# Performance work log

Hardware: AMD Instinct MI355X
Metric: run time of the kernel (lower is better)

Reference implementation:

```python
import jax, jax.numpy as jnp
import numpy as np

B, S, D = 2, 2048, 2048
E, K, F = 8, 2, 4096
EPS_LN = 1e-5
EPS_AUX = 1e-9


def setup_inputs() -> dict:
    key = jax.random.key(0)
    ks = jax.random.split(key, 12)
    s_d = 1.0 / np.sqrt(D)
    s_f = 1.0 / np.sqrt(F)
    return {
        "x": jax.random.normal(ks[0], (B, S, D), dtype=jnp.float32),
        # router LayerNorm
        "ln_gamma": jnp.ones((D,), jnp.float32),
        "ln_beta": jnp.zeros((D,), jnp.float32),
        # router MLP: Linear(D,D) -> ReLU -> Linear(D,E)
        "rW1": jax.random.uniform(ks[1], (D, D), jnp.float32, -s_d, s_d),
        "rb1": jnp.zeros((D,), jnp.float32),
        "rW2": jax.random.uniform(ks[2], (D, E), jnp.float32, -s_d, s_d),
        "rb2": jnp.zeros((E,), jnp.float32),
        # experts: per-expert FFN D -> F -> D
        "We1": jax.random.uniform(ks[3], (E, D, F), jnp.float32, -s_d, s_d),
        "be1": jnp.zeros((E, F), jnp.float32),
        "We2": jax.random.uniform(ks[4], (E, F, D), jnp.float32, -s_f, s_f),
        "be2": jnp.zeros((E, D), jnp.float32),
    }


def _layer_norm(x, gamma, beta):
    mu = jnp.mean(x, axis=-1, keepdims=True)
    var = jnp.mean(jnp.square(x - mu), axis=-1, keepdims=True)
    return (x - mu) * jax.lax.rsqrt(var + EPS_LN) * gamma + beta


def reference(x, ln_gamma, ln_beta, rW1, rb1, rW2, rb2, We1, be1, We2, be2):
    # --- BaseRouter ---
    x_norm = _layer_norm(x, ln_gamma, ln_beta)
    h = jax.nn.relu(jnp.einsum("bsd,de->bse", x_norm, rW1) + rb1)
    router_logits = jnp.einsum("bsd,de->bse", h, rW2) + rb2  # [B,S,E]
    router_probs = jax.nn.softmax(router_logits, axis=-1)

    top_k_probs, top_k_indices = jax.lax.top_k(router_probs, K)  # [B,S,K]
    top_k_probs = top_k_probs / jnp.sum(top_k_probs, axis=-1, keepdims=True)

    # aux load-balance loss (detached in original via .item())
    p_mean = jnp.mean(router_probs, axis=(0, 1))  # [E]
    aux_loss = jnp.sum(p_mean * jnp.log(p_mean * E + EPS_AUX))

    # --- dispatch / combine weights: scatter top-k probs to [B,S,E] ---
    one_hot = jax.nn.one_hot(top_k_indices, E, dtype=x.dtype)  # [B,S,K,E]
    combine = jnp.einsum("bske,bsk->bse", one_hot, top_k_probs)  # [B,S,E]

    # --- experts: dense per-expert FFN, weighted combine ---
    eh = jax.nn.relu(jnp.einsum("bsd,edf->ebsf", x, We1) + be1[:, None, None, :])
    ey = jnp.einsum("ebsf,efd->ebsd", eh, We2) + be2[:, None, None, :]
    out = jnp.einsum("ebsd,bse->bsd", ey, combine)

    return out, aux_loss
```

## Files before the change

kernel.cpp:

```cpp
#include <hip/hip_runtime.h>
#include <hip/hip_bf16.h>

#define NTOK 4096
#define DIM  2048
#define NEXP 8
#define FDIM 4096
#define NPAIR 8192

typedef __attribute__((ext_vector_type(4))) float     f32x4;
typedef __attribute__((ext_vector_type(8))) short     s16x8;
typedef __attribute__((ext_vector_type(4))) short     s16x4;
typedef __attribute__((ext_vector_type(8))) _Float16  f16x8;
typedef __attribute__((ext_vector_type(4))) _Float16  f16x4;

#define DEVI static __device__ __forceinline__

DEVI void gl2lds(const void* g, void* l) {
  __builtin_amdgcn_global_load_lds((const __attribute__((address_space(1))) unsigned int*)g,
                                   (__attribute__((address_space(3))) unsigned int*)l, 16, 0, 0);
}

DEVI float bf2f(unsigned short s) {
  unsigned int u = ((unsigned int)s) << 16; float f; __builtin_memcpy(&f, &u, 4); return f;
}
DEVI unsigned short f2bf(float f) {
  __hip_bfloat16 h = __float2bfloat16(f); unsigned short s; __builtin_memcpy(&s, &h, 2); return s;
}
DEVI float wredsum(float v) {
#pragma unroll
  for (int o = 32; o > 0; o >>= 1) v += __shfl_xor(v, o);
  return v;
}

__global__ __launch_bounds__(256) void ln_conv_kernel(
    const float* __restrict__ x, const float* __restrict__ gamma, const float* __restrict__ beta,
    _Float16* __restrict__ xh, _Float16* __restrict__ xl, unsigned short* __restrict__ xbf)
{
  int tok = blockIdx.x;
  int tid = threadIdx.x, lane = tid & 63, wv = tid >> 6;
  const float* xr = x + (size_t)tok * DIM;
  float v[8];
  *(float4*)(v)     = *(const float4*)(xr + tid * 8);
  *(float4*)(v + 4) = *(const float4*)(xr + tid * 8 + 4);
  float s = v[0]+v[1]+v[2]+v[3]+v[4]+v[5]+v[6]+v[7];
  __shared__ float red[4];
  s = wredsum(s);
  if (lane == 0) red[wv] = s;
  __syncthreads();
  float mu = (red[0]+red[1]+red[2]+red[3]) * (1.f / DIM);
  __syncthreads();
  float s2 = 0.f;
#pragma unroll
  for (int j = 0; j < 8; j++) { float d = v[j] - mu; s2 += d * d; }
  s2 = wredsum(s2);
  if (lane == 0) red[wv] = s2;
  __syncthreads();
  float var = (red[0]+red[1]+red[2]+red[3]) * (1.f / DIM);
  float rs = 1.0f / sqrtf(var + 1e-5f);

  float4 g0 = *(const float4*)(gamma + tid*8), g1 = *(const float4*)(gamma + tid*8 + 4);
  float4 b0 = *(const float4*)(beta  + tid*8), b1 = *(const float4*)(beta  + tid*8 + 4);
  float gg[8] = {g0.x,g0.y,g0.z,g0.w,g1.x,g1.y,g1.z,g1.w};
  float bb[8] = {b0.x,b0.y,b0.z,b0.w,b1.x,b1.y,b1.z,b1.w};
  f16x8 vh, vl; s16x8 vb;
#pragma unroll
  for (int j = 0; j < 8; j++) {
    float xn = (v[j] - mu) * rs * gg[j] + bb[j];
    _Float16 h = (_Float16)xn;
    vh[j] = h;
    vl[j] = (_Float16)((xn - (float)h) * 4096.f);
    vb[j] = (short)f2bf(v[j]);
  }
  *(f16x8*)(xh + (size_t)tok*DIM + tid*8) = vh;
  *(f16x8*)(xl + (size_t)tok*DIM + tid*8) = vl;
  *(s16x8*)(xbf + (size_t)tok*DIM + tid*8) = vb;
}

__global__ __launch_bounds__(256) void transpose_bf16_kernel(
    const float* __restrict__ src, unsigned short* __restrict__ dst, int R, int C)
{
  src += (size_t)blockIdx.z * R * C;
  dst += (size_t)blockIdx.z * R * C;
  __shared__ float tile[64][65];
  int r0 = blockIdx.y * 64, c0 = blockIdx.x * 64;
  int tx = threadIdx.x & 15, ty = threadIdx.x >> 4;
#pragma unroll
  for (int i = 0; i < 4; i++) {
    float4 v = *(const float4*)(src + (size_t)(r0 + ty*4 + i) * C + c0 + tx*4);
    tile[ty*4+i][tx*4+0] = v.x; tile[ty*4+i][tx*4+1] = v.y;
    tile[ty*4+i][tx*4+2] = v.z; tile[ty*4+i][tx*4+3] = v.w;
  }
  __syncthreads();
#pragma unroll
  for (int i = 0; i < 4; i++) {
    int c = c0 + ty*4 + i;
    s16x4 o;
    o[0] = (short)f2bf(tile[tx*4+0][ty*4+i]); o[1] = (short)f2bf(tile[tx*4+1][ty*4+i]);
    o[2] = (short)f2bf(tile[tx*4+2][ty*4+i]); o[3] = (short)f2bf(tile[tx*4+3][ty*4+i]);
    *(s16x4*)(dst + (size_t)c * R + r0 + tx*4) = o;
  }
}

__global__ __launch_bounds__(256) void transpose_f16split_kernel(
    const float* __restrict__ src, _Float16* __restrict__ dh, _Float16* __restrict__ dl, int R, int C)
{
  __shared__ float tile[64][65];
  int r0 = blockIdx.y * 64, c0 = blockIdx.x * 64;
  int tx = threadIdx.x & 15, ty = threadIdx.x >> 4;
#pragma unroll
  for (int i = 0; i < 4; i++) {
    float4 v = *(const float4*)(src + (size_t)(r0 + ty*4 + i) * C + c0 + tx*4);
    tile[ty*4+i][tx*4+0] = v.x; tile[ty*4+i][tx*4+1] = v.y;
    tile[ty*4+i][tx*4+2] = v.z; tile[ty*4+i][tx*4+3] = v.w;
  }
  __syncthreads();
#pragma unroll
  for (int i = 0; i < 4; i++) {
    int c = c0 + ty*4 + i;
    f16x4 oh, ol;
#pragma unroll
    for (int j = 0; j < 4; j++) {
      float f = tile[tx*4+j][ty*4+i];
      _Float16 h = (_Float16)f;
      oh[j] = h;
      ol[j] = (_Float16)((f - (float)h) * 4096.f);
    }
    *(f16x4*)(dh + (size_t)c * R + r0 + tx*4) = oh;
    *(f16x4*)(dl + (size_t)c * R + r0 + tx*4) = ol;
  }
}

#define R_TA 10240
#define R_TB 5120
__global__ __launch_bounds__(256) void router_gemm_kernel(
    const _Float16* __restrict__ Ah, const _Float16* __restrict__ Al,
    const _Float16* __restrict__ Bh, const _Float16* __restrict__ Bl,
    const float* __restrict__ bias, float* __restrict__ Cout)
{
  __shared__ char lds[2*R_TA + 2*R_TB];
  char* lAh = lds;             char* lAl = lds + R_TA;
  char* lBh = lds + 2*R_TA;    char* lBl = lds + 2*R_TA + R_TB;
  const int K = DIM;
  int m0 = blockIdx.y * 128, n0 = blockIdx.x * 64;
  int tid = threadIdx.x, lane = tid & 63, wv = tid >> 6;
  int wm = wv >> 1, wn = wv & 1;

  const char* srcAh[3]; const char* srcAl[3];
  const char* srcBh[2]; const char* srcBl[2];
  {
    int i = 0;
    for (int c = wv; c < 10; c += 4, i++) {
      int doff = c*1024 + lane*16;
      int row = doff / 80; int b = doff - row*80; if (b >= 64) b = 0;
      srcAh[i] = (const char*)(Ah + (size_t)(m0+row)*K) + b;
      srcAl[i] = (const char*)(Al + (size_t)(m0+row)*K) + b;
    }
    i = 0;
    for (int c = wv; c < 5; c += 4, i++) {
      int doff = c*1024 + lane*16;
      int row = doff / 80; int b = doff - row*80; if (b >= 64) b = 0;
      srcBh[i] = (const char*)(Bh + (size_t)(n0+row)*K) + b;
      srcBl[i] = (const char*)(Bl + (size_t)(n0+row)*K) + b;
    }
  }

  f32x4 acc1[4][2], acc2[4][2];
#pragma unroll
  for (int mb = 0; mb < 4; mb++)
#pragma unroll
    for (int nb = 0; nb < 2; nb++) {
      acc1[mb][nb] = (f32x4){0.f,0.f,0.f,0.f};
      acc2[mb][nb] = (f32x4){0.f,0.f,0.f,0.f};
    }

  for (int kt = 0; kt < K/32; kt++) {
    {
      int i = 0;
      for (int c = wv; c < 10; c += 4, i++) {
        gl2lds(srcAh[i], lAh + c*1024);
        gl2lds(srcAl[i], lAl + c*1024);
        srcAh[i] += 64; srcAl[i] += 64;
      }
      i = 0;
      for (int c = wv; c < 5; c += 4, i++) {
        gl2lds(srcBh[i], lBh + c*1024);
        gl2lds(srcBl[i], lBl + c*1024);
        srcBh[i] += 64; srcBl[i] += 64;
      }
    }
    __syncthreads();
    int kb = (lane >> 4) * 16;
    f16x8 ah[4], al[4], bh[2], bl[2];
#pragma unroll
    for (int mb = 0; mb < 4; mb++) {
      int r = wm*64 + mb*16 + (lane & 15);
      ah[mb] = *(const f16x8*)(lAh + r*80 + kb);
      al[mb] = *(const f16x8*)(lAl + r*80 + kb);
    }
#pragma unroll
    for (int nb = 0; nb < 2; nb++) {
      int r = wn*32 + nb*16 + (lane & 15);
      bh[nb] = *(const f16x8*)(lBh + r*80 + kb);
      bl[nb] = *(const f16x8*)(lBl + r*80 + kb);
    }
#pragma unroll
    for (int mb = 0; mb < 4; mb++)
#pragma unroll
      for (int nb = 0; nb < 2; nb++) {
        acc1[mb][nb] = __builtin_amdgcn_mfma_f32_16x16x32_f16(ah[mb], bh[nb], acc1[mb][nb], 0,0,0);
        acc2[mb][nb] = __builtin_amdgcn_mfma_f32_16x16x32_f16(ah[mb], bl[nb], acc2[mb][nb], 0,0,0);
        acc2[mb][nb] = __builtin_amdgcn_mfma_f32_16x16x32_f16(al[mb], bh[nb], acc2[mb][nb], 0,0,0);
      }
    __syncthreads();
  }
#pragma unroll
  for (int mb = 0; mb < 4; mb++)
#pragma unroll
    for (int nb = 0; nb < 2; nb++) {
      int col = n0 + wn*32 + nb*16 + (lane & 15);
      float bv = bias[col];
#pragma unroll
      for (int r = 0; r < 4; r++) {
        int m = m0 + wm*64 + mb*16 + (lane >> 4)*4 + r;
        float hval = acc1[mb][nb][r] + acc2[mb][nb][r] * (1.f/4096.f) + bv;
        Cout[(size_t)m*DIM + col] = fmaxf(hval, 0.f);
      }
    }
}

__global__ __launch_bounds__(256) void router_logits_kernel(
    const float* __restrict__ h, const float* __restrict__ rW2, const float* __restrict__ rb2,
    float* __restrict__ probs,
    int* __restrict__ eid, float* __restrict__ wts)
{
  int lane = threadIdx.x & 63, wv = threadIdx.x >> 6;
  int tok = blockIdx.x * 4 + wv;
  const float* hr = h + (size_t)tok * DIM;
  float lg[8] = {0,0,0,0,0,0,0,0};
#pragma unroll
  for (int j = 0; j < 8; j++) {
    int k = j * 256 + lane * 4;
    float4 hv = *(const float4*)(hr + k);
    float hv4[4] = {hv.x, hv.y, hv.z, hv.w};
#pragma unroll
    for (int r = 0; r < 4; r++) {
      const float4* w4 = (const float4*)(rW2 + (size_t)(k + r) * NEXP);
      float4 wa = w4[0], wb = w4[1];
      lg[0] += hv4[r]*wa.x; lg[1] += hv4[r]*wa.y; lg[2] += hv4[r]*wa.z; lg[3] += hv4[r]*wa.w;
      lg[4] += hv4[r]*wb.x; lg[5] += hv4[r]*wb.y; lg[6] += hv4[r]*wb.z; lg[7] += hv4[r]*wb.w;
    }
  }
#pragma unroll
  for (int e = 0; e < 8; e++) {
#pragma unroll
    for (int o = 32; o > 0; o >>= 1) lg[e] += __shfl_xor(lg[e], o);
  }
  if (lane == 0) {
    float l[8], p[8];
    float m = -1e30f;
#pragma unroll
    for (int e = 0; e < 8; e++) { l[e] = lg[e] + rb2[e]; m = fmaxf(m, l[e]); }
    float s = 0.f;
#pragma unroll
    for (int e = 0; e < 8; e++) { p[e] = expf(l[e] - m); s += p[e]; }
    float inv = 1.f / s;
#pragma unroll
    for (int e = 0; e < 8; e++) { p[e] *= inv; probs[(size_t)tok*8 + e] = p[e]; }
    int i0 = 0;
#pragma unroll
    for (int e = 1; e < 8; e++) if (p[e] > p[i0]) i0 = e;
    int i1 = (i0 == 0) ? 1 : 0;
#pragma unroll
    for (int e = 0; e < 8; e++) if (e != i0 && p[e] > p[i1]) i1 = e;
    float denom = 1.f / (p[i0] + p[i1]);
    eid[tok*2+0] = i0; eid[tok*2+1] = i1;
    wts[tok*2+0] = p[i0]*denom; wts[tok*2+1] = p[i1]*denom;
  }
}

__global__ __launch_bounds__(256) void router_sort_kernel(
    const int* __restrict__ eid, const float* __restrict__ probs,
    int* __restrict__ cnt, int* __restrict__ basep,
    int* __restrict__ tokenlist, int* __restrict__ pairslot,
    float* __restrict__ aux_out)
{
  __shared__ int hist[256][8];
  __shared__ float wsum[4][8];
  __shared__ int bl[8];
  __shared__ int lcnt[8];
  int t = threadIdx.x, lane = t & 63, wv = t >> 6;

  int me[32];
  {
    const int4* ep = (const int4*)(eid + t * 32);
#pragma unroll
    for (int q = 0; q < 8; q++) {
      int4 v = ep[q];
      me[q*4+0] = v.x; me[q*4+1] = v.y; me[q*4+2] = v.z; me[q*4+3] = v.w;
    }
  }
#pragma unroll
  for (int e = 0; e < 8; e++) {
    int ce = 0;
#pragma unroll
    for (int i = 0; i < 32; i++) ce += (me[i] == e) ? 1 : 0;
    hist[t][e] = ce;
  }

  float part[8] = {0,0,0,0,0,0,0,0};
  for (int i = 0; i < 16; i++) {
    const float4* p4 = (const float4*)(probs + (size_t)(t*16 + i) * 8);
    float4 a = p4[0], b = p4[1];
    part[0]+=a.x; part[1]+=a.y; part[2]+=a.z; part[3]+=a.w;
    part[4]+=b.x; part[5]+=b.y; part[6]+=b.z; part[7]+=b.w;
  }
#pragma unroll
  for (int e = 0; e < 8; e++) {
#pragma unroll
    for (int o = 32; o > 0; o >>= 1) part[e] += __shfl_xor(part[e], o);
  }
  if (lane == 0) {
#pragma unroll
    for (int e = 0; e < 8; e++) wsum[wv][e] = part[e];
  }
  __syncthreads();

  if (t < 8) {
    int running = 0;
    for (int i = 0; i < 256; i++) { int tmp = hist[i][t]; hist[i][t] = running; running += tmp; }
    lcnt[t] = running;
  }
  __syncthreads();
  if (t == 0) {
    int b = 0; float aux = 0.f;
#pragma unroll
    for (int e = 0; e < 8; e++) {
      int ce = lcnt[e];
      bl[e] = b; basep[e] = b; cnt[e] = ce; b += ce;
      float pm = (wsum[0][e]+wsum[1][e]+wsum[2][e]+wsum[3][e]) * (1.f / NTOK);
      aux += pm * logf(pm * 8.f + 1e-9f);
    }
    *aux_out = aux;
  }
  __syncthreads();

#pragma unroll
  for (int i = 0; i < 32; i++) {
    int e = me[i];
    int r = 0;
#pragma unroll
    for (int j = 0; j < i; j++) r += (me[j] == e) ? 1 : 0;
    int slot = bl[e] + hist[t][e] + r;
    int pair = t*32 + i;
    tokenlist[slot] = pair >> 1;
    pairslot[pair] = slot;
  }
}

#define E_TILE 18432
template<int MODE>
__global__ __launch_bounds__(256) void expert_gemm_kernel(
    const unsigned short* __restrict__ Abase,
    const unsigned short* __restrict__ Bbase,
    const float* __restrict__ bias,
    unsigned short* __restrict__ Cout,
    const int* __restrict__ cnt, const int* __restrict__ basep,
    const int* __restrict__ tokenlist)
{
  const int K = (MODE == 1) ? DIM : FDIM;
  const int N = (MODE == 1) ? FDIM : DIM;
  int e = blockIdx.y >> 5, mt = blockIdx.y & 31;
  int ne = cnt[e];
  if (mt * 128 >= ne) return;
  int mbase = basep[e] + mt * 128;
  int n0 = blockIdx.x * 128;
  __shared__ char lds[2 * E_TILE];
  char* lA = lds; char* lB = lds + E_TILE;
  int tid = threadIdx.x, lane = tid & 63, wv = tid >> 6;
  int wm = wv >> 1, wn = wv & 1;

  const char* srcA[5]; const char* srcB[5];
  {
    int i = 0;
    for (int c = wv; c < 18; c += 4, i++) {
      int doff = c*1024 + lane*16;
      int row = doff / 144; int b = doff - row*144; if (b >= 128) b = 0;
      size_t arow;
      if (MODE == 1) {
        int slot = mbase + row; if (slot > NPAIR - 1) slot = NPAIR - 1;
        arow = (size_t)tokenlist[slot];
      } else {
        arow = (size_t)(mbase + row);
      }
      srcA[i] = (const char*)(Abase + arow * K) + b;
      srcB[i] = (const char*)(Bbase + ((size_t)e * N + n0 + row) * K) + b;
    }
  }

  f32x4 acc[4][4];
#pragma unroll
  for (int mb = 0; mb < 4; mb++)
#pragma unroll
    for (int nb = 0; nb < 4; nb++) acc[mb][nb] = (f32x4){0.f,0.f,0.f,0.f};

  for (int kt = 0; kt < K/64; kt++) {
    {
      int i = 0;
      for (int c = wv; c < 18; c += 4, i++) {
        gl2lds(srcA[i], lA + c*1024);
        gl2lds(srcB[i], lB + c*1024);
        srcA[i] += 128; srcB[i] += 128;
      }
    }
    __syncthreads();
#pragma unroll
    for (int ks = 0; ks < 2; ks++) {
      int kb = ks*64 + (lane >> 4) * 16;
      s16x8 af[4], bf[4];
#pragma unroll
      for (int mb = 0; mb < 4; mb++)
        af[mb] = *(const s16x8*)(lA + (wm*64 + mb*16 + (lane & 15))*144 + kb);
#pragma unroll
      for (int nb = 0; nb < 4; nb++)
        bf[nb] = *(const s16x8*)(lB + (wn*64 + nb*16 + (lane & 15))*144 + kb);
#pragma unroll
      for (int mb = 0; mb < 4; mb++)
#pragma unroll
        for (int nb = 0; nb < 4; nb++)
          acc[mb][nb] = __builtin_amdgcn_mfma_f32_16x16x32_bf16(af[mb], bf[nb], acc[mb][nb], 0,0,0);
    }
    __syncthreads();
  }

#pragma unroll
  for (int mb = 0; mb < 4; mb++)
#pragma unroll
    for (int nb = 0; nb < 4; nb++) {
      int col = n0 + wn*64 + nb*16 + (lane & 15);
      float bv = bias[(size_t)e * N + col];
#pragma unroll
      for (int r = 0; r < 4; r++) {
        int mloc = mt*128 + wm*64 + mb*16 + (lane >> 4)*4 + r;
        if (mloc < ne) {
          float v = acc[mb][nb][r] + bv;
          if (MODE == 1) v = fmaxf(v, 0.f);
          Cout[((size_t)basep[e] + mloc) * N + col] = f2bf(v);
        }
      }
    }
}

__global__ __launch_bounds__(256) void combine_kernel(
    const unsigned short* __restrict__ Yg, const int* __restrict__ pairslot,
    const float* __restrict__ wts, float* __restrict__ out)
{
  int tok = blockIdx.x, tid = threadIdx.x;
  int s0 = pairslot[tok*2], s1 = pairslot[tok*2+1];
  float w0 = wts[tok*2], w1 = wts[tok*2+1];
  s16x8 a = *(const s16x8*)(Yg + (size_t)s0 * DIM + tid*8);
  s16x8 b = *(const s16x8*)(Yg + (size_t)s1 * DIM + tid*8);
  float o[8];
#pragma unroll
  for (int j = 0; j < 8; j++)
    o[j] = w0 * bf2f((unsigned short)a[j]) + w1 * bf2f((unsigned short)b[j]);
  float* op = out + (size_t)tok * DIM + tid*8;
  float4 o0; o0.x=o[0]; o0.y=o[1]; o0.z=o[2]; o0.w=o[3];
  float4 o1; o1.x=o[4]; o1.y=o[5]; o1.z=o[6]; o1.w=o[7];
  *(float4*)op = o0;
  *(float4*)(op + 4) = o1;
}

extern "C" void kernel_launch(void* const* d_in, const int* in_sizes, int n_in,
                              void* d_out, int out_size, void* d_ws, size_t ws_size,
                              hipStream_t stream)
{
  (void)in_sizes; (void)n_in; (void)out_size; (void)ws_size;
  const float* x    = (const float*)d_in[0];
  const float* ln_g = (const float*)d_in[1];
  const float* ln_b = (const float*)d_in[2];
  const float* rW1  = (const float*)d_in[3];
  const float* rb1  = (const float*)d_in[4];
  const float* rW2  = (const float*)d_in[5];
  const float* rb2  = (const float*)d_in[6];
  const float* We1  = (const float*)d_in[7];
  const float* be1  = (const float*)d_in[8];
  const float* We2  = (const float*)d_in[9];
  const float* be2  = (const float*)d_in[10];
  float* out = (float*)d_out;
  float* aux_out = out + (size_t)NTOK * DIM;

  char* ws = (char*)d_ws;
  size_t off = 0;
  auto alloc = [&](size_t bytes) { char* p = ws + off; off += (bytes + 255) & ~(size_t)255; return p; };

  _Float16* XH   = (_Float16*)alloc((size_t)NTOK * DIM * 2);
  _Float16* XL   = (_Float16*)alloc((size_t)NTOK * DIM * 2);
  unsigned short* XBF = (unsigned short*)alloc((size_t)NTOK * DIM * 2);
  _Float16* RW1H = (_Float16*)alloc((size_t)DIM * DIM * 2);
  _Float16* RW1L = (_Float16*)alloc((size_t)DIM * DIM * 2);
  unsigned short* WET = (unsigned short*)alloc((size_t)NEXP * FDIM * DIM * 2);
  unsigned short* EH  = (unsigned short*)alloc((size_t)(NPAIR + 128) * FDIM * 2);
  char* HY = alloc((size_t)(NPAIR + 128) * DIM * 2 > (size_t)NTOK*DIM*4
                     ? (size_t)(NPAIR + 128) * DIM * 2 : (size_t)NTOK*DIM*4);
  float* H = (float*)HY;
  unsigned short* YG = (unsigned short*)HY;
  float* PROB = (float*)alloc((size_t)NTOK * 8 * 4);
  int* CNT  = (int*)alloc(256);
  int* BASE = CNT + 16;
  int* EID  = (int*)alloc((size_t)NPAIR * 4);
  float* WTS = (float*)alloc((size_t)NPAIR * 4);
  int* PAIRSLOT = (int*)alloc((size_t)NPAIR * 4);
  int* TOKLIST  = (int*)alloc((size_t)(NPAIR + 128) * 4);

  ln_conv_kernel<<<NTOK, 256, 0, stream>>>(x, ln_g, ln_b, XH, XL, XBF);
  transpose_f16split_kernel<<<dim3(DIM/64, DIM/64), 256, 0, stream>>>(rW1, RW1H, RW1L, DIM, DIM);
  transpose_bf16_kernel<<<dim3(FDIM/64, DIM/64, NEXP), 256, 0, stream>>>(We1, WET, DIM, FDIM);
  router_gemm_kernel<<<dim3(DIM/64, NTOK/128), 256, 0, stream>>>(XH, XL, RW1H, RW1L, rb1, H);
  router_logits_kernel<<<NTOK/4, 256, 0, stream>>>(H, rW2, rb2, PROB, EID, WTS);
  router_sort_kernel<<<1, 256, 0, stream>>>(EID, PROB, CNT, BASE, TOKLIST, PAIRSLOT, aux_out);
  expert_gemm_kernel<1><<<dim3(FDIM/128, NEXP*32), 256, 0, stream>>>(XBF, WET, be1, EH, CNT, BASE, TOKLIST);
  transpose_bf16_kernel<<<dim3(DIM/64, FDIM/64, NEXP), 256, 0, stream>>>(We2, WET, FDIM, DIM);
  expert_gemm_kernel<2><<<dim3(DIM/128, NEXP*32), 256, 0, stream>>>(EH, WET, be2, YG, CNT, BASE, TOKLIST);
  combine_kernel<<<NTOK, 256, 0, stream>>>(YG, PAIRSLOT, WTS, out);
}
```

Before: 898.2 us.

## Double-buffer expert GEMM LDS tiles with XOR swizzle and prefetch

Rewrites the expert GEMM main loop to double-buffer A/B tiles in 64KB of LDS, issuing global-to-LDS loads for the next K tile before computing on the current one. The padded 144-byte row layout is replaced by a 128-byte row layout with an XOR swizzle to avoid bank conflicts. The two per-iteration barriers become a single barrier with explicit waitcnts, and launch bounds request two blocks per CU. The aim is to overlap memory latency with MFMA work, at the cost of higher LDS use that may limit occupancy.

New measurement: 838.8 us. 1.07x faster.

```diff
diff --git a/kernel.cpp b/kernel.cpp
--- a/kernel.cpp
+++ b/kernel.cpp
@@ -357,9 +357,8 @@
   }
 }
 
-#define E_TILE 18432
 template<int MODE>
-__global__ __launch_bounds__(256) void expert_gemm_kernel(
+__global__ __launch_bounds__(256, 2) void expert_gemm_v3(
     const unsigned short* __restrict__ Abase,
     const unsigned short* __restrict__ Bbase,
     const float* __restrict__ bias,
@@ -369,67 +368,76 @@
 {
   const int K = (MODE == 1) ? DIM : FDIM;
   const int N = (MODE == 1) ? FDIM : DIM;
+  __shared__ char lds[65536];
   int e = blockIdx.y >> 5, mt = blockIdx.y & 31;
   int ne = cnt[e];
   if (mt * 128 >= ne) return;
   int mbase = basep[e] + mt * 128;
   int n0 = blockIdx.x * 128;
-  __shared__ char lds[2 * E_TILE];
-  char* lA = lds; char* lB = lds + E_TILE;
   int tid = threadIdx.x, lane = tid & 63, wv = tid >> 6;
   int wm = wv >> 1, wn = wv & 1;
 
-  const char* srcA[5]; const char* srcB[5];
-  {
-    int i = 0;
-    for (int c = wv; c < 18; c += 4, i++) {
-      int doff = c*1024 + lane*16;
-      int row = doff / 144; int b = doff - row*144; if (b >= 128) b = 0;
-      size_t arow;
-      if (MODE == 1) {
-        int slot = mbase + row; if (slot > NPAIR - 1) slot = NPAIR - 1;
-        arow = (size_t)tokenlist[slot];
-      } else {
-        arow = (size_t)(mbase + row);
+  const char* srcA[4]; const char* srcB[4];
+  int sb = (((lane & 7) ^ ((lane >> 3) & 7)) << 4);
+#pragma unroll
+  for (int i = 0; i < 4; i++) {
+    int c = wv + i*4;
+    int row = c*8 + (lane >> 3);
+    int slot = mbase + row; if (slot > NPAIR - 1) slot = NPAIR - 1;
+    size_t arow = (MODE == 1) ? (size_t)tokenlist[slot] : (size_t)slot;
+    srcA[i] = (const char*)(Abase + arow * K) + sb;
+    srcB[i] = (const char*)(Bbase + ((size_t)e * N + n0 + row) * K) + sb;
+  }
+
+  f32x4 acc[4][4];
+#pragma unroll
+  for (int mb = 0; mb < 4; mb++)
+#pragma unroll
+    for (int nb = 0; nb < 4; nb++) acc[mb][nb] = (f32x4){0.f,0.f,0.f,0.f};
+
+#pragma unroll
+  for (int i = 0; i < 4; i++) {
+    gl2lds(srcA[i], lds + (wv + i*4)*1024);
+    gl2lds(srcB[i], lds + 16384 + (wv + i*4)*1024);
+  }
+  asm volatile("s_waitcnt vmcnt(0)\n\ts_barrier" ::: "memory");
+
+  const int NT = K / 64;
+  int rsw = (lane & 7) << 4;
+  int cur = 0;
+  for (int kt = 0; kt < NT; kt++) {
+    char* cA = lds + cur*32768;
+    char* cB = cA + 16384;
+    if (kt + 1 < NT) {
+      char* nA = lds + (cur^1)*32768;
+      char* nB = nA + 16384;
+      size_t ko = (size_t)(kt + 1) * 128;
+#pragma unroll
+      for (int i = 0; i < 4; i++) {
+        gl2lds(srcA[i] + ko, nA + (wv + i*4)*1024);
+        gl2lds(srcB[i] + ko, nB + (wv + i*4)*1024);
       }
-      srcA[i] = (const char*)(Abase + arow * K) + b;
-      srcB[i] = (const char*)(Bbase + ((size_t)e * N + n0 + row) * K) + b;
-    }
-  }
-
-  f32x4 acc[4][4];
-#pragma unroll
-  for (int mb = 0; mb < 4; mb++)
-#pragma unroll
-    for (int nb = 0; nb < 4; nb++) acc[mb][nb] = (f32x4){0.f,0.f,0.f,0.f};
-
-  for (int kt = 0; kt < K/64; kt++) {
-    {
-      int i = 0;
-      for (int c = wv; c < 18; c += 4, i++) {
-        gl2lds(srcA[i], lA + c*1024);
-        gl2lds(srcB[i], lB + c*1024);
-        srcA[i] += 128; srcB[i] += 128;
-      }
-    }
-    __syncthreads();
+    }
 #pragma unroll
     for (int ks = 0; ks < 2; ks++) {
-      int kb = ks*64 + (lane >> 4) * 16;
+      int kb = (ks*64 + (lane >> 4)*16) ^ rsw;
       s16x8 af[4], bf[4];
 #pragma unroll
       for (int mb = 0; mb < 4; mb++)
-        af[mb] = *(const s16x8*)(lA + (wm*64 + mb*16 + (lane & 15))*144 + kb);
+        af[mb] = *(const s16x8*)(cA + (wm*64 + mb*16 + (lane & 15))*128 + kb);
 #pragma unroll
       for (int nb = 0; nb < 4; nb++)
-        bf[nb] = *(const s16x8*)(lB + (wn*64 + nb*16 + (lane & 15))*144 + kb);
+        bf[nb] = *(const s16x8*)(cB + (wn*64 + nb*16 + (lane & 15))*128 + kb);
 #pragma unroll
       for (int mb = 0; mb < 4; mb++)
 #pragma unroll
         for (int nb = 0; nb < 4; nb++)
           acc[mb][nb] = __builtin_amdgcn_mfma_f32_16x16x32_bf16(af[mb], bf[nb], acc[mb][nb], 0,0,0);
     }
-    __syncthreads();
+    __builtin_amdgcn_sched_barrier(0);
+    asm volatile("s_waitcnt lgkmcnt(0)\n\ts_waitcnt vmcnt(0)\n\ts_barrier" ::: "memory");
+    __builtin_amdgcn_sched_barrier(0);
+    cur ^= 1;
   }
 
 #pragma unroll
@@ -518,8 +526,8 @@
   router_gemm_kernel<<<dim3(DIM/64, NTOK/128), 256, 0, stream>>>(XH, XL, RW1H, RW1L, rb1, H);
   router_logits_kernel<<<NTOK/4, 256, 0, stream>>>(H, rW2, rb2, PROB, EID, WTS);
   router_sort_kernel<<<1, 256, 0, stream>>>(EID, PROB, CNT, BASE, TOKLIST, PAIRSLOT, aux_out);
-  expert_gemm_kernel<1><<<dim3(FDIM/128, NEXP*32), 256, 0, stream>>>(XBF, WET, be1, EH, CNT, BASE, TOKLIST);
+  expert_gemm_v3<1><<<dim3(FDIM/128, NEXP*32), 256, 0, stream>>>(XBF, WET, be1, EH, CNT, BASE, TOKLIST);
   transpose_bf16_kernel<<<dim3(DIM/64, FDIM/64, NEXP), 256, 0, stream>>>(We2, WET, FDIM, DIM);
-  expert_gemm_kernel<2><<<dim3(DIM/128, NEXP*32), 256, 0, stream>>>(EH, WET, be2, YG, CNT, BASE, TOKLIST);
+  expert_gemm_v3<2><<<dim3(DIM/128, NEXP*32), 256, 0, stream>>>(EH, WET, be2, YG, CNT, BASE, TOKLIST);
   combine_kernel<<<NTOK, 256, 0, stream>>>(YG, PAIRSLOT, WTS, out);
 }
```
